# Kernel optimization log

Measured on AMD Instinct MI355X. Metric: run time of the kernel, lower is better.

Reference implementation:

```python
import jax, jax.numpy as jnp
import numpy as np

TEMPERATURE = 0.07
EPS = 1e-8


def setup_inputs() -> dict:
    key = jax.random.key(0)
    k1, k2 = jax.random.split(key)
    B, D = 8192, 256
    embeddings = jax.random.normal(k1, (B, D), dtype=jnp.float32)
    labels = jax.random.randint(k2, (B,), 0, 6, dtype=jnp.int64)
    return {"embeddings": embeddings, "labels": labels}


def reference(embeddings, labels):
    B = embeddings.shape[0]
    # F.normalize(p=2, dim=1): x / max(||x||, eps)
    norm = jnp.linalg.norm(embeddings, axis=1, keepdims=True)
    en = embeddings / jnp.maximum(norm, 1e-12)
    sim = en @ en.T  # [B, B]
    s = sim / TEMPERATURE

    eye = jnp.eye(B, dtype=bool)
    same = labels[:, None] == labels[None, :]
    pos_mask = same & ~eye            # [B, B]
    neg_mask = (~same) & ~eye         # [B, B]

    exp_s = jnp.exp(s)
    # per-row sum of exp over negatives (matches inner-loop denominator term)
    neg_sum = jnp.sum(jnp.where(neg_mask, exp_s, 0.0), axis=1)  # [B]

    # rows contribute only if they have >=1 positive AND >=1 negative
    row_valid = (pos_mask.sum(axis=1) > 0) & (neg_mask.sum(axis=1) > 0)
    pair_mask = pos_mask & row_valid[:, None]

    # -log( exp(s_ij) / (exp(s_ij) + neg_sum_i + 1e-8) ) per positive pair
    per_pair = -jnp.log(exp_s / (exp_s + neg_sum[:, None] + EPS))
    total = jnp.sum(jnp.where(pair_mask, per_pair, 0.0))
    count = jnp.sum(pair_mask)
    loss = jnp.where(count > 0, total / jnp.maximum(count, 1).astype(total.dtype), 0.0)
    return loss
```

## Files before the change

kernel.cpp:

```cpp
#include <hip/hip_runtime.h>
#include <hip/hip_bf16.h>

#define B_ 8192
#define D_ 256
#define TINV 14.285714285714285f
#define EPS_ 1e-8f
#define BK 32
#define NBLK 32
#define NT 64
#define NTRI (NT*(NT+1)/2)

typedef short short8 __attribute__((ext_vector_type(8)));
typedef float f32x4 __attribute__((ext_vector_type(4)));

__device__ __forceinline__ void mfma_bf16(f32x4& acc, short8 a, short8 b) {
    asm("v_mfma_f32_16x16x32_bf16 %0, %1, %2, %0" : "+v"(acc) : "v"(a), "v"(b));
}

__device__ __forceinline__ void mfma_fence() {
    __builtin_amdgcn_sched_barrier(0);
    asm volatile("s_nop 7\ns_nop 7" ::);
}

__device__ __forceinline__ unsigned short f2bf(float x) {
    __hip_bfloat16 h = __float2bfloat16(x);
    return __builtin_bit_cast(unsigned short, h);
}

__device__ __forceinline__ void tri_decode(int idx, int& bi, int& bj) {
    int t = NTRI - 1 - idx;
    int u = (int)((sqrtf(8.f * (float)t + 1.f) - 1.f) * 0.5f);
    while (u * (u + 1) / 2 > t) --u;
    while ((u + 1) * (u + 2) / 2 <= t) ++u;
    bi = (NT - 1) - u;
    bj = (NT - 1) - (t - u * (u + 1) / 2);
}

__device__ __forceinline__ void stage(const char* gbase, int row0, int k0,
                                      short* ldst, int lane, int wid) {
    int p = (wid << 6) + lane;
    int row = p >> 2;
    int kb = (p & 3) ^ ((row >> 1) & 3);
    const char* g = gbase + ((size_t)(row0 + row) * (D_ * 2) + (size_t)(k0 + kb * 8) * 2);
    __builtin_amdgcn_global_load_lds(
        (const __attribute__((address_space(1))) unsigned int*)g,
        (__attribute__((address_space(3))) unsigned int*)(ldst + ((size_t)wid << 9)),
        16, 0, 0);
}

__device__ __forceinline__ void compute_step(const short* lA, const short* lB,
                                             int lane, int wm, int wn, f32x4 acc[2][4]) {
    int rl = lane & 15, kb = lane >> 4;
    short8 a[2];
#pragma unroll
    for (int m = 0; m < 2; ++m) {
        int row = wm * 32 + m * 16 + rl;
        a[m] = ((const short8*)lA)[row * 4 + (kb ^ ((row >> 1) & 3))];
    }
#pragma unroll
    for (int n = 0; n < 4; ++n) {
        int row = wn * 64 + n * 16 + rl;
        short8 b = ((const short8*)lB)[row * 4 + (kb ^ ((row >> 1) & 3))];
        mfma_bf16(acc[0][n], a[0], b);
        mfma_bf16(acc[1][n], a[1], b);
    }
}

#define PIPE_STEP(T, WAITS)                                                     \
    {                                                                           \
        asm volatile(WAITS ::: "memory");                                       \
        __builtin_amdgcn_sched_barrier(0);                                      \
        __builtin_amdgcn_s_barrier();                                           \
        __builtin_amdgcn_sched_barrier(0);                                      \
        if ((T) + 2 < 8) {                                                      \
            stage(enb, i0, ((T) + 2) * BK, lA[((T) + 2) % 3], lane, wid);       \
            stage(enb, j0, ((T) + 2) * BK, lB[((T) + 2) % 3], lane, wid);       \
        }                                                                       \
        compute_step(lA[(T) % 3], lB[(T) % 3], lane, wm, wn, acc);              \
    }

__device__ __forceinline__ void gemm_pipe(const char* enb, int i0, int j0,
                                          short (*lA)[128 * BK], short (*lB)[128 * BK],
                                          int lane, int wid, int wm, int wn,
                                          f32x4 acc[2][4]) {
    stage(enb, i0, 0, lA[0], lane, wid);
    stage(enb, j0, 0, lB[0], lane, wid);
    stage(enb, i0, BK, lA[1], lane, wid);
    stage(enb, j0, BK, lB[1], lane, wid);
    PIPE_STEP(0, "s_waitcnt vmcnt(2)")
    PIPE_STEP(1, "s_waitcnt vmcnt(2)")
    PIPE_STEP(2, "s_waitcnt vmcnt(2)")
    PIPE_STEP(3, "s_waitcnt vmcnt(2)")
    PIPE_STEP(4, "s_waitcnt vmcnt(2)")
    PIPE_STEP(5, "s_waitcnt vmcnt(2)")
    PIPE_STEP(6, "s_waitcnt vmcnt(2)")
    PIPE_STEP(7, "s_waitcnt vmcnt(0)")
    mfma_fence();
}

__global__ __launch_bounds__(256) void k_bhist(const int* __restrict__ labels,
                                               unsigned* __restrict__ blockhist,
                                               float* __restrict__ negsum,
                                               float* __restrict__ total) {
    __shared__ unsigned h[8];
    int b = blockIdx.x, t = threadIdx.x;
    if (t < 8) h[t] = 0;
    negsum[b * 256 + t] = 0.f;
    if (b == 0 && t == 0) *total = 0.f;
    __syncthreads();
    atomicAdd(&h[labels[b * 256 + t] & 7], 1u);
    __syncthreads();
    if (t < 8) blockhist[b * 8 + t] = h[t];
}

__global__ __launch_bounds__(256) void k_pos(const int* __restrict__ labels,
                                             const unsigned* __restrict__ blockhist,
                                             unsigned* __restrict__ hist,
                                             int* __restrict__ pos) {
    __shared__ unsigned cnt[8][NBLK];
    __shared__ unsigned clsbase[8];
    __shared__ unsigned wcnt[4][8];
    int b = blockIdx.x, t = threadIdx.x;
    { int bb = t >> 3, c = t & 7; cnt[c][bb] = blockhist[bb * 8 + c]; }
    __syncthreads();
    if (t < 8) {
        unsigned run = 0;
        for (int b2 = 0; b2 < NBLK; ++b2) {
            unsigned v = cnt[t][b2];
            cnt[t][b2] = run;
            run += v;
        }
        clsbase[t] = run;
        if (b == 0) hist[t] = run;
    }
    __syncthreads();
    if (t == 0) {
        unsigned run = 0;
        for (int c = 0; c < 8; ++c) {
            unsigned tot = clsbase[c];
            clsbase[c] = run;
            run += tot;
        }
    }
    __syncthreads();
    int row = b * 256 + t;
    int c = labels[row] & 7;
    int lane = t & 63, w = t >> 6;
    unsigned long long lanebelow = (1ull << lane) - 1ull;
    unsigned myrank = 0;
#pragma unroll
    for (int cv = 0; cv < 8; ++cv) {
        unsigned long long mask = __ballot(c == cv);
        if (lane == 0) wcnt[w][cv] = (unsigned)__popcll(mask);
        if (c == cv) myrank = (unsigned)__popcll(mask & lanebelow);
    }
    __syncthreads();
    unsigned pre = 0;
    for (int wp = 0; wp < 4; ++wp) if (wp < w) pre += wcnt[wp][c];
    pos[row] = (int)(clsbase[c] + cnt[c][b] + pre + myrank);
}

__global__ __launch_bounds__(256) void k_scatter(const float* __restrict__ emb,
                                                 const int* __restrict__ labels,
                                                 const int* __restrict__ pos,
                                                 __hip_bfloat16* __restrict__ en_s,
                                                 int* __restrict__ lab_s) {
    int row = blockIdx.x * 4 + (threadIdx.x >> 6);
    int lane = threadIdx.x & 63;
    float4 v = reinterpret_cast<const float4*>(emb)[(size_t)row * 64 + lane];
    float ss = v.x * v.x + v.y * v.y + v.z * v.z + v.w * v.w;
#pragma unroll
    for (int off = 32; off >= 1; off >>= 1) ss += __shfl_xor(ss, off, 64);
    float scale = 1.0f / fmaxf(sqrtf(ss), 1e-12f);
    int p = pos[row];
    ushort4 o;
    o.x = f2bf(v.x * scale);
    o.y = f2bf(v.y * scale);
    o.z = f2bf(v.z * scale);
    o.w = f2bf(v.w * scale);
    reinterpret_cast<ushort4*>(en_s)[(size_t)p * 64 + lane] = o;
    if (lane == 0) lab_s[p] = labels[row] & 7;
}

template <bool USEP>
__global__ __launch_bounds__(512, 8) void k_negsum(const __hip_bfloat16* __restrict__ en,
                                                   const int* __restrict__ lab_s,
                                                   float* __restrict__ P,
                                                   float* __restrict__ negsum) {
    __shared__ short lA[3][128 * BK];
    __shared__ short lB[3][128 * BK];
    int bi, bj;
    tri_decode(blockIdx.x, bi, bj);
    int i0 = bi * 128, j0 = bj * 128;
    int tid = threadIdx.x;
    int lane = tid & 63, wid = tid >> 6;
    int wm = wid >> 1, wn = wid & 1;
    int rl = lane & 15, rowg = (lane >> 4) * 4;
    const char* enb = (const char*)en;

    int lj[4], li[2][4];
#pragma unroll
    for (int n = 0; n < 4; ++n) lj[n] = lab_s[j0 + wn * 64 + n * 16 + rl];
#pragma unroll
    for (int m = 0; m < 2; ++m)
#pragma unroll
        for (int r = 0; r < 4; ++r) li[m][r] = lab_s[i0 + wm * 32 + m * 16 + rowg + r];

    f32x4 acc[2][4] = {};
    stage(enb, i0, 0, lA[0], lane, wid);
    stage(enb, j0, 0, lB[0], lane, wid);
    stage(enb, i0, BK, lA[1], lane, wid);
    stage(enb, j0, BK, lB[1], lane, wid);
    PIPE_STEP(0, "s_waitcnt vmcnt(2)")
    PIPE_STEP(1, "s_waitcnt vmcnt(2)")
    PIPE_STEP(2, "s_waitcnt vmcnt(2)")
    PIPE_STEP(3, "s_waitcnt vmcnt(2)")
    PIPE_STEP(4, "s_waitcnt vmcnt(2)")
    PIPE_STEP(5, "s_waitcnt vmcnt(2)")
    PIPE_STEP(6, "s_waitcnt vmcnt(2)")
    PIPE_STEP(7, "s_waitcnt vmcnt(0)")
    mfma_fence();

    float* sredR = (float*)lA;
    float* sredC = (float*)lB;

    float cp[4] = {0.f, 0.f, 0.f, 0.f};
#pragma unroll
    for (int m = 0; m < 2; ++m) {
        float part[4];
#pragma unroll
        for (int r = 0; r < 4; ++r) {
            part[r] = 0.f;
#pragma unroll
            for (int n = 0; n < 4; ++n) {
                float e = (li[m][r] != lj[n]) ? __expf(acc[m][n][r] * TINV) : 0.f;
                part[r] += e;
                cp[n] += e;
            }
        }
#pragma unroll
        for (int off = 1; off < 16; off <<= 1)
#pragma unroll
            for (int r = 0; r < 4; ++r) part[r] += __shfl_xor(part[r], off, 64);
        if (rl == 0) {
#pragma unroll
            for (int r = 0; r < 4; ++r) {
                int row = wm * 32 + m * 16 + rowg + r;
                if (USEP) sredR[wn * 128 + row] = part[r];
                else      atomicAdd(&negsum[i0 + row], part[r]);
            }
        }
    }
    if (bi != bj) {
#pragma unroll
        for (int n = 0; n < 4; ++n) {
            cp[n] += __shfl_xor(cp[n], 16, 64);
            cp[n] += __shfl_xor(cp[n], 32, 64);
            if (lane < 16) {
                int col = wn * 64 + n * 16 + lane;
                if (USEP) sredC[wm * 128 + col] = cp[n];
                else      atomicAdd(&negsum[j0 + col], cp[n]);
            }
        }
    }
    if (USEP) {
        __syncthreads();
        if (tid < 128)
            P[(size_t)bj * B_ + i0 + tid] = sredR[tid] + sredR[128 + tid];
        else if (tid < 256 && bi != bj) {
            int c = tid - 128;
            P[(size_t)bi * B_ + j0 + c] =
                sredC[c] + sredC[128 + c] + sredC[256 + c] + sredC[384 + c];
        }
    }
}

__global__ __launch_bounds__(256) void k_red(const float* __restrict__ P,
                                             float* __restrict__ negsum) {
    int i = blockIdx.x * 256 + threadIdx.x;
    float s = 0.f;
#pragma unroll 8
    for (int k = 0; k < 64; ++k) s += P[(size_t)k * B_ + i];
    negsum[i] = s;
}

__global__ __launch_bounds__(512, 8) void k_pairs(const __hip_bfloat16* __restrict__ en,
                                                  const int* __restrict__ lab_s,
                                                  const float* __restrict__ negsum,
                                                  const unsigned* __restrict__ hist,
                                                  float* __restrict__ total) {
    int bi, bj;
    tri_decode(blockIdx.x, bi, bj);
    int i0 = bi * 128, j0 = bj * 128;
    if (lab_s[j0] > lab_s[i0 + 127]) return;

    __shared__ short lA[3][128 * BK];
    __shared__ short lB[3][128 * BK];
    __shared__ int sLi[128], sLj[128];
    __shared__ float sNgI[128], sNgJ[128];
    int tid = threadIdx.x;
    if (tid < 128) {
        int l = lab_s[i0 + tid];
        unsigned h = hist[l];
        sLi[tid] = (h > 1u && h < (unsigned)B_) ? l : -1;
        sNgI[tid] = negsum[i0 + tid] + EPS_;
    } else if (tid < 256) {
        int idx = tid - 128;
        int l = lab_s[j0 + idx];
        unsigned h = hist[l];
        sLj[idx] = (h > 1u && h < (unsigned)B_) ? l : -1;
        sNgJ[idx] = negsum[j0 + idx] + EPS_;
    }
    __syncthreads();

    int lane = tid & 63, wid = tid >> 6;
    int wm = wid >> 1, wn = wid & 1;
    f32x4 acc[2][4] = {};
    gemm_pipe((const char*)en, i0, j0, lA, lB, lane, wid, wm, wn, acc);

    int rl = lane & 15, rowg = (lane >> 4) * 4;
    int lj[4];
    float ngJ[4];
#pragma unroll
    for (int n = 0; n < 4; ++n) {
        lj[n] = sLj[wn * 64 + n * 16 + rl];
        ngJ[n] = sNgJ[wn * 64 + n * 16 + rl];
    }

    bool offd = (bi != bj);
    float tot = 0.f;
#pragma unroll
    for (int m = 0; m < 2; ++m) {
#pragma unroll
        for (int r = 0; r < 4; ++r) {
            int ii = wm * 32 + m * 16 + rowg + r;
            int li = sLi[ii];
            float ngI = sNgI[ii];
#pragma unroll
            for (int n = 0; n < 4; ++n) {
                int jj = wn * 64 + n * 16 + rl;
                bool use = (li == lj[n]) && (li >= 0) && (offd || ii != jj);
                if (use) {
                    float s = acc[m][n][r] * TINV;
                    float e = __expf(s);
                    float t = __logf(e + ngI) - s;
                    if (offd) t += __logf(e + ngJ[n]) - s;
                    tot += t;
                }
            }
        }
    }
#pragma unroll
    for (int off = 32; off >= 1; off >>= 1) tot += __shfl_xor(tot, off, 64);
    __shared__ float sred[8];
    if (lane == 0) sred[wid] = tot;
    __syncthreads();
    if (tid == 0) {
        float s = 0.f;
#pragma unroll
        for (int w = 0; w < 8; ++w) s += sred[w];
        atomicAdd(total, s);
    }
}

__global__ __launch_bounds__(64) void k_final(const unsigned* __restrict__ hist,
                                              const float* __restrict__ total,
                                              float* __restrict__ out) {
    int t = threadIdx.x;
    unsigned c = 0;
    if (t < 8) {
        unsigned h = hist[t];
        if (h > 1u && h < (unsigned)B_) c = h * (h - 1u);
    }
#pragma unroll
    for (int off = 4; off >= 1; off >>= 1) c += (unsigned)__shfl_xor((int)c, off, 64);
    if (t == 0) out[0] = (c > 0u) ? total[0] / (float)c : 0.f;
}

extern "C" void kernel_launch(void* const* d_in, const int* in_sizes, int n_in,
                              void* d_out, int out_size, void* d_ws, size_t ws_size,
                              hipStream_t stream) {
    const float* emb = (const float*)d_in[0];
    const int* labels = (const int*)d_in[1];
    float* out = (float*)d_out;
    char* ws = (char*)d_ws;

    const size_t EN_BYTES = (size_t)B_ * D_ * 2;
    __hip_bfloat16* en_s = (__hip_bfloat16*)ws;
    char* p = ws + EN_BYTES;
    float* negsum = (float*)p;            p += (size_t)B_ * 4;
    int* lab_s = (int*)p;                 p += (size_t)B_ * 4;
    int* pos = (int*)p;                   p += (size_t)B_ * 4;
    unsigned* blockhist = (unsigned*)p;   p += NBLK * 8 * 4;
    unsigned* hist = (unsigned*)p;        p += 64;
    float* total = (float*)p;             p += 64;
    float* P = (float*)p;
    size_t need = (size_t)(p - ws) + (size_t)NT * B_ * 4;
    bool bigws = ws_size >= need;

    k_bhist<<<NBLK, 256, 0, stream>>>(labels, blockhist, negsum, total);
    k_pos<<<NBLK, 256, 0, stream>>>(labels, blockhist, hist, pos);
    k_scatter<<<B_ / 4, 256, 0, stream>>>(emb, labels, pos, en_s, lab_s);
    if (bigws) {
        k_negsum<true><<<NTRI, 512, 0, stream>>>(en_s, lab_s, P, negsum);
        k_red<<<B_ / 256, 256, 0, stream>>>(P, negsum);
    } else {
        k_negsum<false><<<NTRI, 512, 0, stream>>>(en_s, lab_s, P, negsum);
    }
    k_pairs<<<NTRI, 512, 0, stream>>>(en_s, lab_s, negsum, hist, total);
    k_final<<<1, 64, 0, stream>>>(hist, total, out);
}
```

Before: 72.63 us.

## Use 256x128 panel tiles with 1024-thread blocks in negsum kernel

Reworks the negsum GEMM so each block covers a 256-row panel against a 128-column tile with 16 waves, instead of 128x128 triangular tiles with 8 waves. The B tile in LDS is shared across twice as many rows, cutting global loads of the column operand and the block count (1056 instead of 2080). Diagonal-straddling panels compute some redundant tiles, and masking logic decides which row and column partial sums are written. The larger LDS footprint and 1024-thread blocks may reduce occupancy, and only the first 8 waves stage the B tile, so the two wave groups use different vmcnt waits.

```diff
diff --git a/kernel.cpp b/kernel.cpp
--- a/kernel.cpp
+++ b/kernel.cpp
@@ -9,6 +9,7 @@
 #define NBLK 32
 #define NT 64
 #define NTRI (NT*(NT+1)/2)
+#define NGB 1056
 
 typedef short short8 __attribute__((ext_vector_type(8)));
 typedef float f32x4 __attribute__((ext_vector_type(4)));
@@ -34,6 +35,18 @@
     while ((u + 1) * (u + 2) / 2 <= t) ++u;
     bi = (NT - 1) - u;
     bj = (NT - 1) - (t - u * (u + 1) / 2);
+}
+
+__device__ __forceinline__ void panel_decode(int idx, int& p, int& bj) {
+    int rem = idx, pp = 0;
+    for (;;) {
+        int nc = 64 - 2 * pp;
+        if (rem < nc) break;
+        rem -= nc;
+        ++pp;
+    }
+    p = pp;
+    bj = 2 * pp + rem;
 }
 
 __device__ __forceinline__ void stage(const char* gbase, int row0, int k0,
@@ -75,6 +88,20 @@
         if ((T) + 2 < 8) {                                                      \
             stage(enb, i0, ((T) + 2) * BK, lA[((T) + 2) % 3], lane, wid);       \
             stage(enb, j0, ((T) + 2) * BK, lB[((T) + 2) % 3], lane, wid);       \
+        }                                                                       \
+        compute_step(lA[(T) % 3], lB[(T) % 3], lane, wm, wn, acc);              \
+    }
+
+#define NSTEP(T, WU, WL)                                                        \
+    {                                                                           \
+        if (wid < 8) { asm volatile("s_waitcnt vmcnt(" WU ")" ::: "memory"); }  \
+        else         { asm volatile("s_waitcnt vmcnt(" WL ")" ::: "memory"); }  \
+        __builtin_amdgcn_sched_barrier(0);                                      \
+        __builtin_amdgcn_s_barrier();                                           \
+        __builtin_amdgcn_sched_barrier(0);                                      \
+        if ((T) + 2 < 8) {                                                      \
+            stage(enb, i0, ((T) + 2) * BK, lA[((T) + 2) % 3], lane, wid);       \
+            if (wid < 8) stage(enb, j0, ((T) + 2) * BK, lB[((T) + 2) % 3], lane, wid); \
         }                                                                       \
         compute_step(lA[(T) % 3], lB[(T) % 3], lane, wm, wn, acc);              \
     }
@@ -183,15 +210,15 @@
 }
 
 template <bool USEP>
-__global__ __launch_bounds__(512, 8) void k_negsum(const __hip_bfloat16* __restrict__ en,
-                                                   const int* __restrict__ lab_s,
-                                                   float* __restrict__ P,
-                                                   float* __restrict__ negsum) {
-    __shared__ short lA[3][128 * BK];
+__global__ __launch_bounds__(1024, 8) void k_negsum(const __hip_bfloat16* __restrict__ en,
+                                                    const int* __restrict__ lab_s,
+                                                    float* __restrict__ P,
+                                                    float* __restrict__ negsum) {
+    __shared__ short lA[3][256 * BK];
     __shared__ short lB[3][128 * BK];
-    int bi, bj;
-    tri_decode(blockIdx.x, bi, bj);
-    int i0 = bi * 128, j0 = bj * 128;
+    int p, bj;
+    panel_decode(blockIdx.x, p, bj);
+    int i0 = p * 256, j0 = bj * 128;
     int tid = threadIdx.x;
     int lane = tid & 63, wid = tid >> 6;
     int wm = wid >> 1, wn = wid & 1;
@@ -208,18 +235,25 @@
 
     f32x4 acc[2][4] = {};
     stage(enb, i0, 0, lA[0], lane, wid);
-    stage(enb, j0, 0, lB[0], lane, wid);
+    if (wid < 8) stage(enb, j0, 0, lB[0], lane, wid);
     stage(enb, i0, BK, lA[1], lane, wid);
-    stage(enb, j0, BK, lB[1], lane, wid);
-    PIPE_STEP(0, "s_waitcnt vmcnt(2)")
-    PIPE_STEP(1, "s_waitcnt vmcnt(2)")
-    PIPE_STEP(2, "s_waitcnt vmcnt(2)")
-    PIPE_STEP(3, "s_waitcnt vmcnt(2)")
-    PIPE_STEP(4, "s_waitcnt vmcnt(2)")
-    PIPE_STEP(5, "s_waitcnt vmcnt(2)")
-    PIPE_STEP(6, "s_waitcnt vmcnt(2)")
-    PIPE_STEP(7, "s_waitcnt vmcnt(0)")
+    if (wid < 8) stage(enb, j0, BK, lB[1], lane, wid);
+    NSTEP(0, "2", "1")
+    NSTEP(1, "2", "1")
+    NSTEP(2, "2", "1")
+    NSTEP(3, "2", "1")
+    NSTEP(4, "2", "1")
+    NSTEP(5, "2", "1")
+    NSTEP(6, "2", "1")
+    NSTEP(7, "0", "0")
     mfma_fence();
+
+    bool isU = (wm < 4);
+    bool doUblk = (bj != 2 * p + 1);
+    bool colU = (bj >= 2 * p + 2);
+    bool colL = (bj != 2 * p + 1);
+    bool doRow = isU ? doUblk : true;
+    bool doCol = isU ? colU : colL;
 
     float* sredR = (float*)lA;
     float* sredC = (float*)lB;
@@ -242,16 +276,16 @@
         for (int off = 1; off < 16; off <<= 1)
 #pragma unroll
             for (int r = 0; r < 4; ++r) part[r] += __shfl_xor(part[r], off, 64);
-        if (rl == 0) {
+        if (rl == 0 && doRow) {
 #pragma unroll
             for (int r = 0; r < 4; ++r) {
                 int row = wm * 32 + m * 16 + rowg + r;
-                if (USEP) sredR[wn * 128 + row] = part[r];
+                if (USEP) sredR[wn * 256 + row] = part[r];
                 else      atomicAdd(&negsum[i0 + row], part[r]);
             }
         }
     }
-    if (bi != bj) {
+    if (doCol) {
 #pragma unroll
         for (int n = 0; n < 4; ++n) {
             cp[n] += __shfl_xor(cp[n], 16, 64);
@@ -265,12 +299,19 @@
     }
     if (USEP) {
         __syncthreads();
-        if (tid < 128)
-            P[(size_t)bj * B_ + i0 + tid] = sredR[tid] + sredR[128 + tid];
-        else if (tid < 256 && bi != bj) {
-            int c = tid - 128;
-            P[(size_t)bi * B_ + j0 + c] =
-                sredC[c] + sredC[128 + c] + sredC[256 + c] + sredC[384 + c];
+        if (tid < 256) {
+            if (tid >= 128 || doUblk)
+                P[(size_t)bj * B_ + i0 + tid] = sredR[tid] + sredR[256 + tid];
+        } else if (tid < 384) {
+            int c = tid - 256;
+            if (colU)
+                P[(size_t)(2 * p) * B_ + j0 + c] =
+                    sredC[c] + sredC[128 + c] + sredC[256 + c] + sredC[384 + c];
+        } else if (tid < 512) {
+            int c = tid - 384;
+            if (colL)
+                P[(size_t)(2 * p + 1) * B_ + j0 + c] =
+                    sredC[512 + c] + sredC[640 + c] + sredC[768 + c] + sredC[896 + c];
         }
     }
 }
@@ -402,10 +443,10 @@
     k_pos<<<NBLK, 256, 0, stream>>>(labels, blockhist, hist, pos);
     k_scatter<<<B_ / 4, 256, 0, stream>>>(emb, labels, pos, en_s, lab_s);
     if (bigws) {
-        k_negsum<true><<<NTRI, 512, 0, stream>>>(en_s, lab_s, P, negsum);
+        k_negsum<true><<<NGB, 1024, 0, stream>>>(en_s, lab_s, P, negsum);
         k_red<<<B_ / 256, 256, 0, stream>>>(P, negsum);
     } else {
-        k_negsum<false><<<NTRI, 512, 0, stream>>>(en_s, lab_s, P, negsum);
+        k_negsum<false><<<NGB, 1024, 0, stream>>>(en_s, lab_s, P, negsum);
     }
     k_pairs<<<NTRI, 512, 0, stream>>>(en_s, lab_s, negsum, hist, total);
     k_final<<<1, 64, 0, stream>>>(hist, total, out);
```

Result: slower. 78.48 us (+8.1%).
